# Performance work log

Hardware: AMD Instinct MI355X
Metric: run time of the kernel (lower is better)

The kernel has to match this reference:

```python
import jax, jax.numpy as jnp
import numpy as np

N_NODES = 50000
N_EDGES = 800000
NODE_IN = 10
EDGE_IN = 7
H = 128
N_LAYERS = 6
OUT_DIM = 3


def setup_inputs() -> dict:
    key = jax.random.key(0)
    ks = jax.random.split(key, 32)
    s = 0.05
    inp = {
        "x": jax.random.normal(ks[0], (N_NODES, NODE_IN), jnp.float32),
        "edge_attr": jax.random.normal(ks[1], (N_EDGES, EDGE_IN), jnp.float32),
        "edge_index": jax.random.randint(ks[2], (2, N_EDGES), 0, N_NODES, jnp.int32),
        "bc_disp": jax.random.uniform(ks[3], (N_NODES, 1), jnp.float32),
        "bc_rot": jax.random.uniform(ks[4], (N_NODES, 1), jnp.float32),
        # node encoder: MLP(10, [H], H)
        "ne_w1": jax.random.normal(ks[5], (NODE_IN, H), jnp.float32) * s,
        "ne_b1": jnp.zeros((H,), jnp.float32),
        "ne_w2": jax.random.normal(ks[6], (H, H), jnp.float32) * s,
        "ne_b2": jnp.zeros((H,), jnp.float32),
        # edge encoder: MLP(7, [H], H)
        "ee_w1": jax.random.normal(ks[7], (EDGE_IN, H), jnp.float32) * s,
        "ee_b1": jnp.zeros((H,), jnp.float32),
        "ee_w2": jax.random.normal(ks[8], (H, H), jnp.float32) * s,
        "ee_b2": jnp.zeros((H,), jnp.float32),
        # 6 GraphNetworkLayers: edge model (3H -> H), node model (2H -> H)
        "mp_ew": jax.random.normal(ks[9], (N_LAYERS, 3 * H, H), jnp.float32) * s,
        "mp_eb": jnp.zeros((N_LAYERS, H), jnp.float32),
        "mp_nw": jax.random.normal(ks[10], (N_LAYERS, 2 * H, H), jnp.float32) * s,
        "mp_nb": jnp.zeros((N_LAYERS, H), jnp.float32),
        "d_w1": jax.random.normal(ks[11], (H, H), jnp.float32) * s,
        "d_b1": jnp.zeros((H,), jnp.float32),
        "d_w2": jax.random.normal(ks[12], (H, 64), jnp.float32) * s,
        "d_b2": jnp.zeros((64,), jnp.float32),
        "d_w3": jax.random.normal(ks[13], (64, OUT_DIM), jnp.float32) * (s * 5.0),
        "d_b3": jnp.full((OUT_DIM,), 0.5, jnp.float32),
    }
    return inp


def reference(x, edge_attr, edge_index, bc_disp, bc_rot,
              ne_w1, ne_b1, ne_w2, ne_b2,
              ee_w1, ee_b1, ee_w2, ee_b2,
              mp_ew, mp_eb, mp_nw, mp_nb,
              d_w1, d_b1, d_w2, d_b2, d_w3, d_b3):
    # encode nodes and edges (Linear -> ReLU -> Linear)
    h = jax.nn.relu(x @ ne_w1 + ne_b1) @ ne_w2 + ne_b2            # [N, H]
    e = jax.nn.relu(edge_attr @ ee_w1 + ee_b1) @ ee_w2 + ee_b2    # [E, H]
    src = edge_index[0]
    dst = edge_index[1]
    # 6 residual message-passing layers: gather -> edge MLP -> scatter-add -> node MLP
    for l in range(N_LAYERS):
        msg_in = jnp.concatenate([h[src], h[dst], e], axis=-1)    # [E, 3H]
        msg = jax.nn.relu(msg_in @ mp_ew[l] + mp_eb[l])           # [E, H]
        agg = jax.ops.segment_sum(msg, dst, num_segments=N_NODES)  # [N, H] (aggr='add')
        upd = jax.nn.relu(jnp.concatenate([h, agg], axis=-1) @ mp_nw[l] + mp_nb[l])
        h = h + upd                                               # residual
    # decode: Linear -> ReLU -> Linear -> ReLU -> Linear
    z = jax.nn.relu(h @ d_w1 + d_b1)
    z = jax.nn.relu(z @ d_w2 + d_b2)
    pred = z @ d_w3 + d_b3                                        # [N, 3]
    # hard boundary conditions
    pred = jnp.concatenate([pred[:, 0:2] * (1.0 - bc_disp),
                            pred[:, 2:3] * (1.0 - bc_rot)], axis=-1)
    return pred
```

## Files before the change

kernel.cpp:

```cpp
#include <hip/hip_runtime.h>
#include <hip/hip_bf16.h>

#define NN 50000
#define NE 800000
#define H 128

typedef __hip_bfloat16 bf16;
typedef __attribute__((ext_vector_type(8))) short short8v;
typedef __attribute__((ext_vector_type(4))) float f32x4;

static __device__ __forceinline__ unsigned short f2bf_bits(float x) {
  union { __hip_bfloat16 b; unsigned short u; } cv;
  cv.b = __float2bfloat16(x);
  return cv.u;
}

__global__ __launch_bounds__(256) void zero_counts_kernel(int* __restrict__ counts) {
  int i = blockIdx.x * 256 + threadIdx.x;
  if (i < NN) counts[i] = 0;
}

__global__ __launch_bounds__(256) void hist_kernel(const int* __restrict__ dstI,
                                                   int* __restrict__ counts) {
  int e = blockIdx.x * 256 + threadIdx.x;
  if (e < NE) atomicAdd(&counts[dstI[e]], 1);
}

__global__ __launch_bounds__(256) void scan_kernel(const int* __restrict__ counts,
                                                   int* __restrict__ cursor) {
  __shared__ int sdata[256];
  __shared__ int sbase;
  const int t = threadIdx.x;
  if (t == 0) sbase = 0;
  __syncthreads();
  for (int c0 = 0; c0 < NN; c0 += 256) {
    int i = c0 + t;
    int v = (i < NN) ? counts[i] : 0;
    sdata[t] = v;
    __syncthreads();
    #pragma unroll
    for (int off = 1; off < 256; off <<= 1) {
      int x = (t >= off) ? sdata[t - off] : 0;
      __syncthreads();
      sdata[t] += x;
      __syncthreads();
    }
    if (i < NN) cursor[i] = sbase + sdata[t] - v;
    __syncthreads();
    if (t == 255) sbase += sdata[255];
    __syncthreads();
  }
}

__global__ __launch_bounds__(256) void scatter_kernel(
    const float* __restrict__ ea, const int* __restrict__ srcI, const int* __restrict__ dstI,
    int* __restrict__ cursor, bf16* __restrict__ eap,
    int* __restrict__ srcp, int* __restrict__ dstp) {
  int e = blockIdx.x * 256 + threadIdx.x;
  if (e >= NE) return;
  int d = dstI[e];
  int pos = atomicAdd(&cursor[d], 1);
  srcp[pos] = srcI[e];
  dstp[pos] = d;
  #pragma unroll
  for (int k = 0; k < 7; ++k) eap[(size_t)pos * 7 + k] = __float2bfloat16(ea[(size_t)e * 7 + k]);
}

__global__ __launch_bounds__(256) void fuse_w3_kernel(
    const float* __restrict__ ee_w2, const float* __restrict__ ee_b2,
    const float* __restrict__ mp_ew, const float* __restrict__ mp_eb,
    float* __restrict__ W3p, float* __restrict__ c3)
{
  const int l = blockIdx.x >> 3;
  const int cc = (blockIdx.x & 7) * 16;
  __shared__ float sA[H * H];
  __shared__ float sB[H * 16];
  const float* W3 = mp_ew + (size_t)l * 384 * H + 256 * H;
  for (int i = threadIdx.x; i < H * H; i += 256) sA[i] = ee_w2[i];
  for (int i = threadIdx.x; i < H * 16; i += 256) {
    int k = i >> 4, j = i & 15;
    sB[i] = W3[k * H + cc + j];
  }
  __syncthreads();
  float* out = W3p + (size_t)l * H * H;
  for (int i = threadIdx.x; i < H * 16; i += 256) {
    int r = i >> 4, j = i & 15;
    float acc = 0.f;
    #pragma unroll 8
    for (int k = 0; k < H; ++k) acc += sA[r * H + k] * sB[k * 16 + j];
    out[r * H + cc + j] = acc;
  }
  if (threadIdx.x < 16) {
    int j = threadIdx.x;
    float acc = mp_eb[l * H + cc + j];
    for (int k = 0; k < H; ++k) acc += ee_b2[k] * sB[k * 16 + j];
    c3[l * H + cc + j] = acc;
  }
}

__global__ __launch_bounds__(256) void repack_w_kernel(
    const float* __restrict__ src0, size_t lstride, bf16* __restrict__ dst0, int K)
{
  const int l = blockIdx.x;
  const float* src = src0 + (size_t)l * lstride;
  bf16* dst = dst0 + (size_t)l * K * 128;
  const int nkk = K / 32;
  const int nslots = 8 * nkk * 64;
  for (int idx = threadIdx.x; idx < nslots; idx += 256) {
    int ng = idx / (nkk * 64);
    int rem = idx % (nkk * 64);
    int kk = rem / 64, ln = rem % 64;
    #pragma unroll
    for (int j = 0; j < 8; ++j) {
      int k = kk * 32 + ((ln >> 4) * 8) + j;
      int col = ng * 16 + (ln & 15);
      dst[(size_t)idx * 8 + j] = __float2bfloat16(src[(size_t)k * 128 + col]);
    }
  }
}

__global__ __launch_bounds__(256) void node_encoder_kernel(
    const float* __restrict__ in,
    const float* __restrict__ w1, const float* __restrict__ b1,
    const float* __restrict__ w2, const float* __restrict__ b2,
    float* __restrict__ out, int nrows)
{
  __shared__ float sw1[10 * H];
  __shared__ float sw2[H * H];
  __shared__ float sb1[H];
  __shared__ float sb2[H];
  __shared__ float sin_[8][10];
  __shared__ float st[8][H];

  for (int i = threadIdx.x; i < 10 * H; i += 256) sw1[i] = w1[i];
  for (int i = threadIdx.x; i < H * H; i += 256) sw2[i] = w2[i];
  if (threadIdx.x < H) { sb1[threadIdx.x] = b1[threadIdx.x]; sb2[threadIdx.x] = b2[threadIdx.x]; }
  __syncthreads();

  const int c = threadIdx.x & 127;
  const int hf = threadIdx.x >> 7;

  for (long long r0 = (long long)blockIdx.x * 8; r0 < nrows; r0 += (long long)gridDim.x * 8) {
    if (threadIdx.x < 80) {
      int j = threadIdx.x / 10, k = threadIdx.x % 10;
      long long r = r0 + j;
      sin_[j][k] = (r < nrows) ? in[r * 10 + k] : 0.f;
    }
    __syncthreads();
    #pragma unroll
    for (int t = 0; t < 4; ++t) {
      int idx = threadIdx.x + t * 256;
      int j = idx >> 7, k = idx & 127;
      float acc = sb1[k];
      #pragma unroll
      for (int i = 0; i < 10; ++i) acc += sin_[j][i] * sw1[i * H + k];
      st[j][k] = fmaxf(acc, 0.f);
    }
    __syncthreads();
    float a0 = sb2[c], a1 = a0, a2 = a0, a3 = a0;
    #pragma unroll 4
    for (int k4 = 0; k4 < H; k4 += 4) {
      float w0 = sw2[(k4 + 0) * H + c];
      float w1v = sw2[(k4 + 1) * H + c];
      float w2v = sw2[(k4 + 2) * H + c];
      float w3v = sw2[(k4 + 3) * H + c];
      float4 s0 = *(const float4*)&st[hf * 4 + 0][k4];
      float4 s1 = *(const float4*)&st[hf * 4 + 1][k4];
      float4 s2 = *(const float4*)&st[hf * 4 + 2][k4];
      float4 s3 = *(const float4*)&st[hf * 4 + 3][k4];
      a0 += s0.x * w0 + s0.y * w1v + s0.z * w2v + s0.w * w3v;
      a1 += s1.x * w0 + s1.y * w1v + s1.z * w2v + s1.w * w3v;
      a2 += s2.x * w0 + s2.y * w1v + s2.z * w2v + s2.w * w3v;
      a3 += s3.x * w0 + s3.y * w1v + s3.z * w2v + s3.w * w3v;
    }
    float accs[4] = {a0, a1, a2, a3};
    #pragma unroll
    for (int j = 0; j < 4; ++j) {
      long long r = r0 + hf * 4 + j;
      if (r < nrows) out[r * H + c] = accs[j];
    }
    __syncthreads();
  }
}

__global__ __launch_bounds__(512) void node_AB_kernel(
    const float* __restrict__ h, const float* __restrict__ W1f, const float* __restrict__ W2f,
    bf16* __restrict__ A, bf16* __restrict__ B, float* __restrict__ agg, int nrows)
{
  __shared__ float sw1[H * H];
  __shared__ float sw2[H * H];
  __shared__ float sh[16][H];
  for (int i = threadIdx.x; i < H * H; i += 512) { sw1[i] = W1f[i]; sw2[i] = W2f[i]; }
  __syncthreads();
  const int c = threadIdx.x & 127;
  const int q = threadIdx.x >> 7;
  for (long long r0 = (long long)blockIdx.x * 16; r0 < nrows; r0 += (long long)gridDim.x * 16) {
    #pragma unroll
    for (int t = 0; t < 4; ++t) {
      int idx = threadIdx.x + t * 512;
      int j = idx >> 7, k = idx & 127;
      long long r = r0 + j;
      sh[j][k] = (r < nrows) ? h[r * H + k] : 0.f;
    }
    __syncthreads();
    float aA[4] = {0, 0, 0, 0}, aB[4] = {0, 0, 0, 0};
    #pragma unroll 2
    for (int k4 = 0; k4 < H; k4 += 4) {
      float w10 = sw1[(k4 + 0) * H + c], w11 = sw1[(k4 + 1) * H + c];
      float w12 = sw1[(k4 + 2) * H + c], w13 = sw1[(k4 + 3) * H + c];
      float w20 = sw2[(k4 + 0) * H + c], w21 = sw2[(k4 + 1) * H + c];
      float w22 = sw2[(k4 + 2) * H + c], w23 = sw2[(k4 + 3) * H + c];
      #pragma unroll
      for (int j = 0; j < 4; ++j) {
        float4 s = *(const float4*)&sh[q * 4 + j][k4];
        aA[j] += s.x * w10 + s.y * w11 + s.z * w12 + s.w * w13;
        aB[j] += s.x * w20 + s.y * w21 + s.z * w22 + s.w * w23;
      }
    }
    #pragma unroll
    for (int j = 0; j < 4; ++j) {
      long long r = r0 + q * 4 + j;
      if (r < nrows) {
        A[r * H + c] = __float2bfloat16(aA[j]);
        B[r * H + c] = __float2bfloat16(aB[j]);
        agg[r * H + c] = 0.f;
      }
    }
    __syncthreads();
  }
}

__global__ __launch_bounds__(512) void edge_mfma_scatter(
    const bf16* __restrict__ eap,
    const int* __restrict__ srcp, const int* __restrict__ dstp,
    const bf16* __restrict__ A, const bf16* __restrict__ B,
    const float* __restrict__ ew1, const float* __restrict__ eb1,
    const bf16* __restrict__ W3b, const float* __restrict__ c3,
    float* __restrict__ agg, int nE)
{
  __shared__ float sew1[7 * H];
  __shared__ float seb1[H];
  __shared__ float sea[64][8];
  __shared__ int   didx[64];
  __shared__ unsigned int shid[64 * 64];
  __shared__ bf16  sAld[64][136];

  for (int i = threadIdx.x; i < 7 * H; i += 512) sew1[i] = ew1[i];
  if (threadIdx.x < H) seb1[threadIdx.x] = eb1[threadIdx.x];

  const int t = threadIdx.x;
  const int lane = t & 63;
  const int wid = t >> 6;
  const int hm = wid >> 2;
  const int colbase = (wid & 3) * 32;

  short8v bfrag[2][4];
  float c3v[2];
  #pragma unroll
  for (int n = 0; n < 2; ++n) {
    c3v[n] = c3[colbase + n * 16 + (lane & 15)];
    int ng = (colbase >> 4) + n;
    #pragma unroll
    for (int kk = 0; kk < 4; ++kk) {
      const bf16* p = W3b + ((size_t)(ng * 4 + kk) * 64 + lane) * 8;
      bfrag[n][kk] = *(const short8v*)p;
    }
  }
  __syncthreads();

  const long long stride = (long long)gridDim.x * 64;
  const int elA0 = t >> 4;
  const int elA1 = 32 + (t >> 4);
  const int segA = (t & 15) * 8;

  float   pf_ea = 0.f;
  int     pf_d = 0;
  short8v pf_A0, pf_A1;
  long long e0 = (long long)blockIdx.x * 64;
  if (e0 < nE) {
    if (t < 448) pf_ea = __bfloat162float(eap[e0 * 7 + t]);
    if (t < 64)  pf_d = dstp[e0 + t];
    int s0 = srcp[e0 + elA0];
    pf_A0 = *(const short8v*)&A[(size_t)s0 * H + segA];
    int s1 = srcp[e0 + elA1];
    pf_A1 = *(const short8v*)&A[(size_t)s1 * H + segA];
  }

  for (; e0 < nE; e0 += stride) {
    if (t < 448) sea[t / 7][t % 7] = pf_ea;
    if (t < 64)  didx[t] = pf_d;
    *(short8v*)&sAld[elA0][segA] = pf_A0;
    *(short8v*)&sAld[elA1][segA] = pf_A1;
    __syncthreads();

    long long e1 = e0 + stride;
    if (e1 < nE) {
      if (t < 448) pf_ea = __bfloat162float(eap[e1 * 7 + t]);
      if (t < 64)  pf_d = dstp[e1 + t];
      int s0 = srcp[e1 + elA0];
      pf_A0 = *(const short8v*)&A[(size_t)s0 * H + segA];
      int s1 = srcp[e1 + elA1];
      pf_A1 = *(const short8v*)&A[(size_t)s1 * H + segA];
    }

    {
      const int e = t >> 3;
      float r0 = sea[e][0], r1 = sea[e][1], r2 = sea[e][2], r3 = sea[e][3];
      float r4 = sea[e][4], r5 = sea[e][5], r6 = sea[e][6];
      #pragma unroll
      for (int p = 0; p < 8; ++p) {
        int k2 = (t & 7) + 8 * p;
        int k = k2 * 2;
        float a0 = seb1[k], a1 = seb1[k + 1];
        a0 += r0 * sew1[0 * H + k] + r1 * sew1[1 * H + k] + r2 * sew1[2 * H + k]
            + r3 * sew1[3 * H + k] + r4 * sew1[4 * H + k] + r5 * sew1[5 * H + k]
            + r6 * sew1[6 * H + k];
        a1 += r0 * sew1[0 * H + k + 1] + r1 * sew1[1 * H + k + 1] + r2 * sew1[2 * H + k + 1]
            + r3 * sew1[3 * H + k + 1] + r4 * sew1[4 * H + k + 1] + r5 * sew1[5 * H + k + 1]
            + r6 * sew1[6 * H + k + 1];
        a0 = fmaxf(a0, 0.f); a1 = fmaxf(a1, 0.f);
        unsigned int w = (unsigned int)f2bf_bits(a0) | ((unsigned int)f2bf_bits(a1) << 16);
        int off = (e * 256 + k2 * 4) ^ ((e & 7) << 4);
        shid[off >> 2] = w;
      }
    }
    __syncthreads();

    f32x4 acc[2][2];
    const f32x4 z = {0.f, 0.f, 0.f, 0.f};
    acc[0][0] = z; acc[0][1] = z; acc[1][0] = z; acc[1][1] = z;
    #pragma unroll
    for (int m = 0; m < 2; ++m) {
      #pragma unroll
      for (int kk = 0; kk < 4; ++kk) {
        int row = hm * 32 + m * 16 + (lane & 15);
        int off = (row * 256 + kk * 64 + (lane >> 4) * 16) ^ ((row & 7) << 4);
        short8v afrag = *(const short8v*)((const char*)shid + off);
        acc[m][0] = __builtin_amdgcn_mfma_f32_16x16x32_bf16(afrag, bfrag[0][kk], acc[m][0], 0, 0, 0);
        acc[m][1] = __builtin_amdgcn_mfma_f32_16x16x32_bf16(afrag, bfrag[1][kk], acc[m][1], 0, 0, 0);
      }
    }

    const int col0 = colbase + (lane & 15);
    const int col1 = col0 + 16;
    #pragma unroll
    for (int m = 0; m < 2; ++m) {
      float vs0 = 0.f, vs1 = 0.f;
      float b0 = 0.f, b1 = 0.f;
      int dprev = -1;
      #pragma unroll
      for (int r = 0; r < 4; ++r) {
        int el = hm * 32 + m * 16 + (lane >> 4) * 4 + r;
        int d = didx[el];
        if (d != dprev) {
          if (dprev >= 0) {
            atomicAdd(&agg[(size_t)dprev * H + col0], vs0);
            atomicAdd(&agg[(size_t)dprev * H + col1], vs1);
          }
          vs0 = 0.f; vs1 = 0.f;
          b0 = __bfloat162float(B[(size_t)d * H + col0]);
          b1 = __bfloat162float(B[(size_t)d * H + col1]);
          dprev = d;
        }
        float a0v = __bfloat162float(sAld[el][col0]);
        float a1v = __bfloat162float(sAld[el][col1]);
        vs0 += fmaxf(acc[m][0][r] + c3v[0] + a0v + b0, 0.f);
        vs1 += fmaxf(acc[m][1][r] + c3v[1] + a1v + b1, 0.f);
      }
      atomicAdd(&agg[(size_t)dprev * H + col0], vs0);
      atomicAdd(&agg[(size_t)dprev * H + col1], vs1);
    }
    __syncthreads();
  }
}

template<int DO_AB>
__global__ __launch_bounds__(256) void fused_update_kernel(
    float* __restrict__ h, const float* __restrict__ aggin,
    const bf16* __restrict__ Wnb, const float* __restrict__ nb,
    const bf16* __restrict__ W1b, const bf16* __restrict__ W2b,
    bf16* __restrict__ A, bf16* __restrict__ B, float* __restrict__ aggz,
    int nrows)
{
  __shared__ unsigned int sKw[32 * 128];
  unsigned short* shnew = (unsigned short*)sKw;

  const int t = threadIdx.x;
  const int lane = t & 63;
  const int wid = t >> 6;
  const int colbase = wid * 32;

  short8v bU[2][8];
  float nbv[2];
  #pragma unroll
  for (int n = 0; n < 2; ++n) {
    int ng = wid * 2 + n;
    nbv[n] = nb[colbase + n * 16 + (lane & 15)];
    #pragma unroll
    for (int kk = 0; kk < 8; ++kk)
      bU[n][kk] = *(const short8v*)(Wnb + ((size_t)(ng * 8 + kk) * 64 + lane) * 8);
  }

  const int ntiles = (nrows + 31) / 32;
  for (int tile = blockIdx.x; tile < ntiles; tile += gridDim.x) {
    const int r0 = tile * 32;
    #pragma unroll
    for (int i = 0; i < 16; ++i) {
      int w = t + i * 256;
      int row = w >> 7, k2 = w & 127;
      int r = r0 + row;
      float v0 = 0.f, v1 = 0.f;
      if (r < nrows) {
        if (k2 < 64) { float2 p = *(const float2*)&h[(size_t)r * H + 2 * k2]; v0 = p.x; v1 = p.y; }
        else         { float2 p = *(const float2*)&aggin[(size_t)r * H + 2 * k2 - 128]; v0 = p.x; v1 = p.y; }
      }
      unsigned int wrd = (unsigned int)f2bf_bits(v0) | ((unsigned int)f2bf_bits(v1) << 16);
      sKw[((w * 4) ^ ((row & 7) << 4)) >> 2] = wrd;
    }
    __syncthreads();

    f32x4 acc[2][2];
    const f32x4 z = {0.f, 0.f, 0.f, 0.f};
    acc[0][0] = z; acc[0][1] = z; acc[1][0] = z; acc[1][1] = z;
    #pragma unroll
    for (int kk = 0; kk < 8; ++kk) {
      #pragma unroll
      for (int m = 0; m < 2; ++m) {
        int row = m * 16 + (lane & 15);
        int off = (row * 512 + kk * 64 + (lane >> 4) * 16) ^ ((row & 7) << 4);
        short8v afrag = *(const short8v*)((const char*)sKw + off);
        acc[m][0] = __builtin_amdgcn_mfma_f32_16x16x32_bf16(afrag, bU[0][kk], acc[m][0], 0, 0, 0);
        acc[m][1] = __builtin_amdgcn_mfma_f32_16x16x32_bf16(afrag, bU[1][kk], acc[m][1], 0, 0, 0);
      }
    }
    __syncthreads();

    #pragma unroll
    for (int m = 0; m < 2; ++m) {
      #pragma unroll
      for (int r = 0; r < 4; ++r) {
        int row = m * 16 + (lane >> 4) * 4 + r;
        int grow = r0 + row;
        #pragma unroll
        for (int n = 0; n < 2; ++n) {
          int col = colbase + n * 16 + (lane & 15);
          float u = fmaxf(acc[m][n][r] + nbv[n], 0.f);
          float hold = (grow < nrows) ? h[(size_t)grow * H + col] : 0.f;
          float hn = hold + u;
          if (grow < nrows) h[(size_t)grow * H + col] = hn;
          if (DO_AB) {
            int i16 = (row * 128 + col) ^ ((row & 7) << 3);
            shnew[i16] = f2bf_bits(hn);
          }
        }
      }
    }

    if (DO_AB) {
      __syncthreads();
      short8v bA[2][4], bB[2][4];
      #pragma unroll
      for (int n = 0; n < 2; ++n) {
        int ng = wid * 2 + n;
        #pragma unroll
        for (int kk = 0; kk < 4; ++kk) {
          bA[n][kk] = *(const short8v*)(W1b + ((size_t)(ng * 4 + kk) * 64 + lane) * 8);
          bB[n][kk] = *(const short8v*)(W2b + ((size_t)(ng * 4 + kk) * 64 + lane) * 8);
        }
      }
      f32x4 aA[2][2], aB2[2][2];
      aA[0][0] = z; aA[0][1] = z; aA[1][0] = z; aA[1][1] = z;
      aB2[0][0] = z; aB2[0][1] = z; aB2[1][0] = z; aB2[1][1] = z;
      #pragma unroll
      for (int kk = 0; kk < 4; ++kk) {
        #pragma unroll
        for (int m = 0; m < 2; ++m) {
          int row = m * 16 + (lane & 15);
          int off = (row * 256 + kk * 64 + (lane >> 4) * 16) ^ ((row & 7) << 4);
          short8v afrag = *(const short8v*)((const char*)shnew + off);
          aA[m][0] = __builtin_amdgcn_mfma_f32_16x16x32_bf16(afrag, bA[0][kk], aA[m][0], 0, 0, 0);
          aA[m][1] = __builtin_amdgcn_mfma_f32_16x16x32_bf16(afrag, bA[1][kk], aA[m][1], 0, 0, 0);
          aB2[m][0] = __builtin_amdgcn_mfma_f32_16x16x32_bf16(afrag, bB[0][kk], aB2[m][0], 0, 0, 0);
          aB2[m][1] = __builtin_amdgcn_mfma_f32_16x16x32_bf16(afrag, bB[1][kk], aB2[m][1], 0, 0, 0);
        }
      }
      #pragma unroll
      for (int m = 0; m < 2; ++m) {
        #pragma unroll
        for (int r = 0; r < 4; ++r) {
          int row = m * 16 + (lane >> 4) * 4 + r;
          int grow = r0 + row;
          if (grow < nrows) {
            #pragma unroll
            for (int n = 0; n < 2; ++n) {
              int col = colbase + n * 16 + (lane & 15);
              A[(size_t)grow * H + col] = __float2bfloat16(aA[m][n][r]);
              B[(size_t)grow * H + col] = __float2bfloat16(aB2[m][n][r]);
              aggz[(size_t)grow * H + col] = 0.f;
            }
          }
        }
      }
    }
    __syncthreads();
  }
}

__global__ __launch_bounds__(512) void decoder_kernel(
    const float* __restrict__ h,
    const float* __restrict__ w1, const float* __restrict__ b1,
    const float* __restrict__ w2, const float* __restrict__ b2,
    const float* __restrict__ w3, const float* __restrict__ b3,
    const float* __restrict__ bcd, const float* __restrict__ bcr,
    float* __restrict__ out, int nrows)
{
  __shared__ float sw1[H * H];
  __shared__ float sw2[H * 64];
  __shared__ float sw3[64 * 3];
  __shared__ float sb1[H], sb2[64], sb3[3];
  __shared__ float sh[16][H], st1[16][H], st2[16][64];
  for (int i = threadIdx.x; i < H * H; i += 512) sw1[i] = w1[i];
  for (int i = threadIdx.x; i < H * 64; i += 512) sw2[i] = w2[i];
  if (threadIdx.x < 64 * 3) sw3[threadIdx.x] = w3[threadIdx.x];
  if (threadIdx.x < H) sb1[threadIdx.x] = b1[threadIdx.x];
  if (threadIdx.x < 64) sb2[threadIdx.x] = b2[threadIdx.x];
  if (threadIdx.x < 3) sb3[threadIdx.x] = b3[threadIdx.x];
  __syncthreads();
  for (long long r0 = (long long)blockIdx.x * 16; r0 < nrows; r0 += (long long)gridDim.x * 16) {
    #pragma unroll
    for (int t = 0; t < 4; ++t) {
      int idx = threadIdx.x + t * 512;
      int j = idx >> 7, k = idx & 127;
      long long r = r0 + j;
      sh[j][k] = (r < nrows) ? h[r * H + k] : 0.f;
    }
    __syncthreads();
    #pragma unroll
    for (int t = 0; t < 4; ++t) {
      int idx = threadIdx.x + t * 512;
      int j = idx >> 7, k = idx & 127;
      float acc = sb1[k];
      #pragma unroll 8
      for (int i = 0; i < H; ++i) acc += sh[j][i] * sw1[i * H + k];
      st1[j][k] = fmaxf(acc, 0.f);
    }
    __syncthreads();
    #pragma unroll
    for (int t = 0; t < 2; ++t) {
      int idx = threadIdx.x + t * 512;
      int j = idx >> 6, k = idx & 63;
      float acc = sb2[k];
      #pragma unroll 8
      for (int i = 0; i < H; ++i) acc += st1[j][i] * sw2[i * 64 + k];
      st2[j][k] = fmaxf(acc, 0.f);
    }
    __syncthreads();
    if (threadIdx.x < 48) {
      int j = threadIdx.x / 3, o = threadIdx.x % 3;
      float acc = sb3[o];
      #pragma unroll 8
      for (int i = 0; i < 64; ++i) acc += st2[j][i] * sw3[i * 3 + o];
      long long r = r0 + j;
      if (r < nrows) {
        float m = (o < 2) ? (1.f - bcd[r]) : (1.f - bcr[r]);
        out[r * 3 + o] = acc * m;
      }
    }
    __syncthreads();
  }
}

extern "C" void kernel_launch(void* const* d_in, const int* in_sizes, int n_in,
                              void* d_out, int out_size, void* d_ws, size_t ws_size,
                              hipStream_t stream) {
  const float* x     = (const float*)d_in[0];
  const float* ea    = (const float*)d_in[1];
  const int*   eidx  = (const int*)d_in[2];
  const float* bcd   = (const float*)d_in[3];
  const float* bcr   = (const float*)d_in[4];
  const float* ne_w1 = (const float*)d_in[5];
  const float* ne_b1 = (const float*)d_in[6];
  const float* ne_w2 = (const float*)d_in[7];
  const float* ne_b2 = (const float*)d_in[8];
  const float* ee_w1 = (const float*)d_in[9];
  const float* ee_b1 = (const float*)d_in[10];
  const float* ee_w2 = (const float*)d_in[11];
  const float* ee_b2 = (const float*)d_in[12];
  const float* mp_ew = (const float*)d_in[13];
  const float* mp_eb = (const float*)d_in[14];
  const float* mp_nw = (const float*)d_in[15];
  const float* mp_nb = (const float*)d_in[16];
  const float* d_w1  = (const float*)d_in[17];
  const float* d_b1  = (const float*)d_in[18];
  const float* d_w2  = (const float*)d_in[19];
  const float* d_b2  = (const float*)d_in[20];
  const float* d_w3  = (const float*)d_in[21];
  const float* d_b3  = (const float*)d_in[22];

  const int* srcI = eidx;
  const int* dstI = eidx + NE;

  char* wsp = (char*)d_ws;
  float* h    = (float*)wsp; wsp += (size_t)NN * H * 4;
  float* agg  = (float*)wsp; wsp += (size_t)NN * H * 4;
  bf16*  A    = (bf16*)wsp;  wsp += (size_t)NN * H * 2;
  bf16*  B    = (bf16*)wsp;  wsp += (size_t)NN * H * 2;
  bf16*  eap  = (bf16*)wsp;  wsp += (size_t)NE * 7 * 2;
  int*   srcp = (int*)wsp;   wsp += (size_t)NE * 4;
  int*   dstp = (int*)wsp;   wsp += (size_t)NE * 4;
  bf16*  W3b  = (bf16*)wsp;  wsp += (size_t)6 * H * H * 2;
  bf16*  Wnb  = (bf16*)wsp;  wsp += (size_t)6 * 256 * H * 2;
  bf16*  W1b  = (bf16*)wsp;  wsp += (size_t)6 * H * H * 2;
  bf16*  W2b  = (bf16*)wsp;  wsp += (size_t)6 * H * H * 2;
  float* c3   = (float*)wsp; wsp += (size_t)6 * H * 4;
  int*   counts = (int*)A;
  int*   cursor = (int*)A + NN;
  float* W3p    = agg;

  zero_counts_kernel<<<(NN + 255) / 256, 256, 0, stream>>>(counts);
  hist_kernel<<<(NE + 255) / 256, 256, 0, stream>>>(dstI, counts);
  scan_kernel<<<1, 256, 0, stream>>>(counts, cursor);
  scatter_kernel<<<(NE + 255) / 256, 256, 0, stream>>>(ea, srcI, dstI, cursor, eap, srcp, dstp);

  fuse_w3_kernel<<<48, 256, 0, stream>>>(ee_w2, ee_b2, mp_ew, mp_eb, W3p, c3);
  repack_w_kernel<<<6, 256, 0, stream>>>(W3p, (size_t)H * H, W3b, 128);
  repack_w_kernel<<<6, 256, 0, stream>>>(mp_nw, (size_t)256 * H, Wnb, 256);
  repack_w_kernel<<<6, 256, 0, stream>>>(mp_ew, (size_t)384 * H, W1b, 128);
  repack_w_kernel<<<6, 256, 0, stream>>>(mp_ew + 128 * H, (size_t)384 * H, W2b, 128);

  node_encoder_kernel<<<2048, 256, 0, stream>>>(x, ne_w1, ne_b1, ne_w2, ne_b2, h, NN);
  node_AB_kernel<<<1024, 512, 0, stream>>>(h, mp_ew, mp_ew + 128 * H, A, B, agg, NN);

  for (int l = 0; l < 6; ++l) {
    edge_mfma_scatter<<<6250, 512, 0, stream>>>(eap, srcp, dstp, A, B, ee_w1, ee_b1,
                                                W3b + (size_t)l * H * H, c3 + l * H, agg, NE);
    if (l < 5) {
      fused_update_kernel<1><<<1563, 256, 0, stream>>>(
          h, agg, Wnb + (size_t)l * 256 * H, mp_nb + l * H,
          W1b + (size_t)(l + 1) * H * H, W2b + (size_t)(l + 1) * H * H,
          A, B, agg, NN);
    } else {
      fused_update_kernel<0><<<1563, 256, 0, stream>>>(
          h, agg, Wnb + (size_t)l * 256 * H, mp_nb + l * H,
          nullptr, nullptr, nullptr, nullptr, nullptr, NN);
    }
  }

  decoder_kernel<<<1024, 512, 0, stream>>>(h, d_w1, d_b1, d_w2, d_b2, d_w3, d_b3,
                                           bcd, bcr, (float*)d_out, NN);
}
```

Baseline: 2.797 ms.

## Parallelize CSR offset scan and hoist AB weight loads out of tile loop

Replaces the single-block serial prefix scan over node counts with a three-pass multi-block scan: per-block sums, a scan of those sums, then per-block local scans with offsets. The W1/W2 bf16 fragment loads in the fused update kernel move out of the per-tile loop so each block loads them once. The fused update grid shrinks from 1563 to 521 blocks, so each block handles about three tiles and the hoisted weight loads are amortized. The cost is more live registers per thread for the hoisted fragments, which could lower occupancy, plus fewer blocks in flight for the update kernel.

```diff
diff --git a/kernel.cpp b/kernel.cpp
--- a/kernel.cpp
+++ b/kernel.cpp
@@ -4,6 +4,7 @@
 #define NN 50000
 #define NE 800000
 #define H 128
+#define NBLK 196
 
 typedef __hip_bfloat16 bf16;
 typedef __attribute__((ext_vector_type(8))) short short8v;
@@ -26,30 +27,52 @@
   if (e < NE) atomicAdd(&counts[dstI[e]], 1);
 }
 
-__global__ __launch_bounds__(256) void scan_kernel(const int* __restrict__ counts,
-                                                   int* __restrict__ cursor) {
+__global__ __launch_bounds__(256) void scan1_kernel(const int* __restrict__ counts,
+                                                    int* __restrict__ bsum) {
   __shared__ int sdata[256];
-  __shared__ int sbase;
+  int i = blockIdx.x * 256 + threadIdx.x;
+  sdata[threadIdx.x] = (i < NN) ? counts[i] : 0;
+  __syncthreads();
+  for (int off = 128; off > 0; off >>= 1) {
+    if (threadIdx.x < off) sdata[threadIdx.x] += sdata[threadIdx.x + off];
+    __syncthreads();
+  }
+  if (threadIdx.x == 0) bsum[blockIdx.x] = sdata[0];
+}
+
+__global__ __launch_bounds__(256) void scan2_kernel(int* __restrict__ bsum) {
+  __shared__ int sdata[256];
   const int t = threadIdx.x;
-  if (t == 0) sbase = 0;
-  __syncthreads();
-  for (int c0 = 0; c0 < NN; c0 += 256) {
-    int i = c0 + t;
-    int v = (i < NN) ? counts[i] : 0;
-    sdata[t] = v;
-    __syncthreads();
-    #pragma unroll
-    for (int off = 1; off < 256; off <<= 1) {
-      int x = (t >= off) ? sdata[t - off] : 0;
-      __syncthreads();
-      sdata[t] += x;
-      __syncthreads();
-    }
-    if (i < NN) cursor[i] = sbase + sdata[t] - v;
-    __syncthreads();
-    if (t == 255) sbase += sdata[255];
-    __syncthreads();
-  }
+  int v = (t < NBLK) ? bsum[t] : 0;
+  sdata[t] = v;
+  __syncthreads();
+  #pragma unroll
+  for (int off = 1; off < 256; off <<= 1) {
+    int x = (t >= off) ? sdata[t - off] : 0;
+    __syncthreads();
+    sdata[t] += x;
+    __syncthreads();
+  }
+  if (t < NBLK) bsum[t] = sdata[t] - v;
+}
+
+__global__ __launch_bounds__(256) void scan3_kernel(const int* __restrict__ counts,
+                                                    const int* __restrict__ bsum,
+                                                    int* __restrict__ cursor) {
+  __shared__ int sdata[256];
+  const int t = threadIdx.x;
+  int i = blockIdx.x * 256 + t;
+  int v = (i < NN) ? counts[i] : 0;
+  sdata[t] = v;
+  __syncthreads();
+  #pragma unroll
+  for (int off = 1; off < 256; off <<= 1) {
+    int x = (t >= off) ? sdata[t - off] : 0;
+    __syncthreads();
+    sdata[t] += x;
+    __syncthreads();
+  }
+  if (i < NN) cursor[i] = bsum[blockIdx.x] + sdata[t] - v;
 }
 
 __global__ __launch_bounds__(256) void scatter_kernel(
@@ -400,6 +423,18 @@
     for (int kk = 0; kk < 8; ++kk)
       bU[n][kk] = *(const short8v*)(Wnb + ((size_t)(ng * 8 + kk) * 64 + lane) * 8);
   }
+  short8v bA[2][4], bB[2][4];
+  if (DO_AB) {
+    #pragma unroll
+    for (int n = 0; n < 2; ++n) {
+      int ng = wid * 2 + n;
+      #pragma unroll
+      for (int kk = 0; kk < 4; ++kk) {
+        bA[n][kk] = *(const short8v*)(W1b + ((size_t)(ng * 4 + kk) * 64 + lane) * 8);
+        bB[n][kk] = *(const short8v*)(W2b + ((size_t)(ng * 4 + kk) * 64 + lane) * 8);
+      }
+    }
+  }
 
   const int ntiles = (nrows + 31) / 32;
   for (int tile = blockIdx.x; tile < ntiles; tile += gridDim.x) {
@@ -458,16 +493,6 @@
 
     if (DO_AB) {
       __syncthreads();
-      short8v bA[2][4], bB[2][4];
-      #pragma unroll
-      for (int n = 0; n < 2; ++n) {
-        int ng = wid * 2 + n;
-        #pragma unroll
-        for (int kk = 0; kk < 4; ++kk) {
-          bA[n][kk] = *(const short8v*)(W1b + ((size_t)(ng * 4 + kk) * 64 + lane) * 8);
-          bB[n][kk] = *(const short8v*)(W2b + ((size_t)(ng * 4 + kk) * 64 + lane) * 8);
-        }
-      }
       f32x4 aA[2][2], aB2[2][2];
       aA[0][0] = z; aA[0][1] = z; aA[1][0] = z; aA[1][1] = z;
       aB2[0][0] = z; aB2[0][1] = z; aB2[1][0] = z; aB2[1][1] = z;
@@ -613,13 +638,16 @@
   bf16*  W1b  = (bf16*)wsp;  wsp += (size_t)6 * H * H * 2;
   bf16*  W2b  = (bf16*)wsp;  wsp += (size_t)6 * H * H * 2;
   float* c3   = (float*)wsp; wsp += (size_t)6 * H * 4;
+  int*   bsum = (int*)wsp;   wsp += 256 * 4;
   int*   counts = (int*)A;
   int*   cursor = (int*)A + NN;
   float* W3p    = agg;
 
   zero_counts_kernel<<<(NN + 255) / 256, 256, 0, stream>>>(counts);
   hist_kernel<<<(NE + 255) / 256, 256, 0, stream>>>(dstI, counts);
-  scan_kernel<<<1, 256, 0, stream>>>(counts, cursor);
+  scan1_kernel<<<NBLK, 256, 0, stream>>>(counts, bsum);
+  scan2_kernel<<<1, 256, 0, stream>>>(bsum);
+  scan3_kernel<<<NBLK, 256, 0, stream>>>(counts, bsum, cursor);
   scatter_kernel<<<(NE + 255) / 256, 256, 0, stream>>>(ea, srcI, dstI, cursor, eap, srcp, dstp);
 
   fuse_w3_kernel<<<48, 256, 0, stream>>>(ee_w2, ee_b2, mp_ew, mp_eb, W3p, c3);
@@ -635,12 +663,12 @@
     edge_mfma_scatter<<<6250, 512, 0, stream>>>(eap, srcp, dstp, A, B, ee_w1, ee_b1,
                                                 W3b + (size_t)l * H * H, c3 + l * H, agg, NE);
     if (l < 5) {
-      fused_update_kernel<1><<<1563, 256, 0, stream>>>(
+      fused_update_kernel<1><<<521, 256, 0, stream>>>(
           h, agg, Wnb + (size_t)l * 256 * H, mp_nb + l * H,
           W1b + (size_t)(l + 1) * H * H, W2b + (size_t)(l + 1) * H * H,
           A, B, agg, NN);
     } else {
-      fused_update_kernel<0><<<1563, 256, 0, stream>>>(
+      fused_update_kernel<0><<<521, 256, 0, stream>>>(
           h, agg, Wnb + (size_t)l * 256 * H, mp_nb + l * H,
           nullptr, nullptr, nullptr, nullptr, nullptr, NN);
     }
```

Result: faster. 2.663 ms (-4.8%).
